# Kernel tuning notes

Measured on AMD Instinct MI355X. Metric: run time of the kernel, lower is better.

Reference implementation:

```python
import jax, jax.numpy as jnp
import numpy as np

CH = 16
R = 9  # reduced_res = ceil(log2(256)+1)


def grid_sample_bilinear(P, gx, gy):
    """torch.F.grid_sample, mode=bilinear, align_corners=True, zeros padding.
    P: (C, H, W); gx indexes width (last axis), gy indexes height. Returns (C, N)."""
    C, H, W = P.shape
    ix = (gx + 1.0) * 0.5 * (W - 1)
    iy = (gy + 1.0) * 0.5 * (H - 1)
    x0 = jnp.floor(ix)
    y0 = jnp.floor(iy)
    wx = ix - x0
    wy = iy - y0
    x0i = jnp.clip(x0.astype(jnp.int32), 0, W - 1)
    x1i = jnp.clip(x0i + 1, 0, W - 1)
    y0i = jnp.clip(y0.astype(jnp.int32), 0, H - 1)
    y1i = jnp.clip(y0i + 1, 0, H - 1)
    v00 = P[:, y0i, x0i]
    v01 = P[:, y0i, x1i]
    v10 = P[:, y1i, x0i]
    v11 = P[:, y1i, x1i]
    return (v00 * (1 - wx) * (1 - wy) + v01 * wx * (1 - wy)
            + v10 * (1 - wx) * wy + v11 * wx * wy)


def plane_feature(P, gx, gy, c_int):
    # sample -> (N, ch, R), then cosine-basis numerical integration over R
    s = grid_sample_bilinear(P, gx, gy)              # (R*ch, N)
    s = s.T.reshape(-1, CH, R)                       # (N, ch, R)
    c = (c_int + 1.0) * 0.5 * (2.0 ** (R - 1) - 1.0)  # (N,)
    freqs = (2.0 ** jnp.arange(R, dtype=jnp.float32)) - 0.5
    basis = jnp.cos(jnp.pi * (c[:, None] + 0.5) * freqs / (2.0 ** R))  # (N, R)
    return 2.0 * jnp.einsum('nr,ncr->nc', basis, s)  # (N, ch)


def setup_inputs() -> dict:
    key = jax.random.key(0)
    k1, k2, k3, k4 = jax.random.split(key, 4)
    coords = jax.random.uniform(k1, (524288, 3), dtype=jnp.float32) * 2.0 - 1.0
    Pu = jax.random.normal(k2, (R * CH, 256, 256), dtype=jnp.float32) * 0.1
    Pv = jax.random.normal(k3, (R * CH, 256, 256), dtype=jnp.float32) * 0.1
    Pw = jax.random.normal(k4, (R * CH, 256, 256), dtype=jnp.float32) * 0.1
    return {"coords": coords, "Pu": Pu, "Pv": Pv, "Pw": Pw}


def reference(coords, Pu, Pv, Pw):
    # Pu sampled with (coord1, coord2), integrated along coord0; etc.
    fu = plane_feature(Pu, coords[:, 1], coords[:, 2], coords[:, 0])
    fv = plane_feature(Pv, coords[:, 0], coords[:, 2], coords[:, 1])
    fw = plane_feature(Pw, coords[:, 0], coords[:, 1], coords[:, 2])
    return fu + fv + fw  # (N, ch)
```

## Files before the change

### kernel.cpp

```cpp
#include <hip/hip_runtime.h>
#include <hip/hip_bf16.h>

#define CHN 16
#define RF 9
#define HWDIM 256
#define POSN (HWDIM * HWDIM)
#define NBINS 32768

__device__ __forceinline__ float bflo(uint32_t v) { return __uint_as_float(v << 16); }
__device__ __forceinline__ float bfhi(uint32_t v) { return __uint_as_float(v & 0xffff0000u); }

__device__ __forceinline__ uint32_t f32_to_bf16(float f) {
    uint32_t u = __float_as_uint(f);
    u += 0x7fffu + ((u >> 16) & 1u);
    return u >> 16;
}

__global__ __launch_bounds__(256) void transpose_pack2(const float* __restrict__ Pu,
                                                       const float* __restrict__ Pv,
                                                       const float* __restrict__ Pw,
                                                       uint4* __restrict__ A,
                                                       uint32_t* __restrict__ B) {
    int tid = blockIdx.x * blockDim.x + threadIdx.x;
    int pos = tid & (POSN - 1);
    int p = tid >> 16;
    const float* P = (p == 0) ? Pu : ((p == 1) ? Pv : Pw);
    uint32_t r8[8];
    uint4* Ap = A + ((size_t)p * POSN + pos) * CHN;
#pragma unroll
    for (int cc = 0; cc < CHN; ++cc) {
        const float* Pc = P + (size_t)(cc * RF) * POSN + pos;
        uint32_t w[4];
#pragma unroll
        for (int j = 0; j < 4; ++j) {
            float v0 = Pc[(size_t)(2 * j) * POSN];
            float v1 = Pc[(size_t)(2 * j + 1) * POSN];
            w[j] = f32_to_bf16(v0) | (f32_to_bf16(v1) << 16);
        }
        Ap[cc] = make_uint4(w[0], w[1], w[2], w[3]);
        uint32_t b8 = f32_to_bf16(Pc[(size_t)8 * POSN]);
        if (cc & 1) r8[cc >> 1] |= (b8 << 16); else r8[cc >> 1] = b8;
    }
    uint32_t* Bp = B + ((size_t)p * POSN + pos) * 8;
#pragma unroll
    for (int j = 0; j < 8; ++j) Bp[j] = r8[j];
}

__device__ __forceinline__ uint32_t part1by2(uint32_t x) {
    x &= 0x3ffu;
    x = (x | (x << 16)) & 0x030000FFu;
    x = (x | (x << 8))  & 0x0300F00Fu;
    x = (x | (x << 4))  & 0x030C30C3u;
    x = (x | (x << 2))  & 0x09249249u;
    return x;
}
__device__ __forceinline__ uint32_t morton_key(float c0, float c1, float c2) {
    int q0 = min(31, max(0, (int)((c0 + 1.f) * 16.f)));
    int q1 = min(31, max(0, (int)((c1 + 1.f) * 16.f)));
    int q2 = min(31, max(0, (int)((c2 + 1.f) * 16.f)));
    return (part1by2((uint32_t)q0) << 2) | (part1by2((uint32_t)q1) << 1) | part1by2((uint32_t)q2);
}

__global__ __launch_bounds__(256) void hist_kernel(const float* __restrict__ coords,
                                                   uint32_t* __restrict__ hist, int N) {
    int n = blockIdx.x * blockDim.x + threadIdx.x;
    if (n >= N) return;
    float c0 = coords[3 * n], c1 = coords[3 * n + 1], c2 = coords[3 * n + 2];
    atomicAdd(&hist[morton_key(c0, c1, c2)], 1u);
}

__global__ __launch_bounds__(1024) void scan_kernel(uint32_t* __restrict__ hist) {
    __shared__ uint32_t part[1024];
    int t = threadIdx.x;
    uint32_t loc[32];
    uint32_t s = 0;
    int base = t * 32;
#pragma unroll
    for (int i = 0; i < 32; ++i) { loc[i] = hist[base + i]; s += loc[i]; }
    part[t] = s;
    __syncthreads();
    for (int off = 1; off < 1024; off <<= 1) {
        uint32_t v = (t >= off) ? part[t - off] : 0u;
        __syncthreads();
        part[t] += v;
        __syncthreads();
    }
    uint32_t run = part[t] - s;
#pragma unroll
    for (int i = 0; i < 32; ++i) { hist[base + i] = run; run += loc[i]; }
}

__global__ __launch_bounds__(256) void scatter_kernel(const float* __restrict__ coords,
                                                      uint32_t* __restrict__ hist,
                                                      float4* __restrict__ sorted, int N) {
    int n = blockIdx.x * blockDim.x + threadIdx.x;
    if (n >= N) return;
    float c0 = coords[3 * n], c1 = coords[3 * n + 1], c2 = coords[3 * n + 2];
    uint32_t key = morton_key(c0, c1, c2);
    uint32_t dst = atomicAdd(&hist[key], 1u);
    sorted[dst] = make_float4(c0, c1, c2, __uint_as_float((uint32_t)n));
}

__global__ __launch_bounds__(256) void triplane_sorted(const float4* __restrict__ sorted,
                                                       const uint4* __restrict__ A,
                                                       const uint32_t* __restrict__ B,
                                                       float* __restrict__ out, int N, int nblk) {
    __shared__ float bas[16][27];
    __shared__ float4 pts[16];
    int blk = blockIdx.x;
    if ((nblk & 7) == 0) {
        int cpx = nblk >> 3;
        blk = (blk & 7) * cpx + (blk >> 3);
    }
    int base = blk * 16;
    int t = threadIdx.x;
    if (t < 16) {
        int i = base + t;
        pts[t] = (i < N) ? sorted[i] : make_float4(0.f, 0.f, 0.f, __uint_as_float(0u));
    }
    __syncthreads();
    if (t < 144) {
        int pt = t / 9, r = t - pt * 9;
        float4 c = pts[pt];
        float k = 3.14159265358979f * ((float)(1 << r) - 0.5f) * (1.f / 512.f);
        bas[pt][0 * 9 + r] = __cosf(((c.x + 1.f) * 127.5f + 0.5f) * k);
        bas[pt][1 * 9 + r] = __cosf(((c.y + 1.f) * 127.5f + 0.5f) * k);
        bas[pt][2 * 9 + r] = __cosf(((c.z + 1.f) * 127.5f + 0.5f) * k);
    }
    __syncthreads();
    int pt = t >> 4, cc = t & 15;
    int gi = base + pt;
    if (gi >= N) return;
    float4 c = pts[pt];
    float acc = 0.f;
#pragma unroll
    for (int p = 0; p < 3; ++p) {
        float gx = (p == 0) ? c.y : c.x;
        float gy = (p == 2) ? c.y : c.z;
        float ix = (gx + 1.f) * 127.5f;
        float iy = (gy + 1.f) * 127.5f;
        float x0f = floorf(ix), y0f = floorf(iy);
        float wx = ix - x0f, wy = iy - y0f;
        int x0 = (int)x0f; x0 = max(0, min(x0, HWDIM - 1));
        int y0 = (int)y0f; y0 = max(0, min(y0, HWDIM - 1));
        int x1 = min(x0 + 1, HWDIM - 1);
        int y1 = min(y0 + 1, HWDIM - 1);
        float b[9];
#pragma unroll
        for (int r = 0; r < 9; ++r) b[r] = bas[pt][p * 9 + r];
        const uint4* Ap = A + (size_t)p * POSN * CHN;
        const uint32_t* Bp = B + (size_t)p * POSN * 8;
        int pos4[4] = { y0 * HWDIM + x0, y0 * HWDIM + x1, y1 * HWDIM + x0, y1 * HWDIM + x1 };
        float w4[4] = { (1.f - wx) * (1.f - wy), wx * (1.f - wy), (1.f - wx) * wy, wx * wy };
        float ps = 0.f;
#pragma unroll
        for (int k = 0; k < 4; ++k) {
            uint4 a = Ap[(size_t)pos4[k] * CHN + cc];
            uint32_t bw = Bp[(size_t)pos4[k] * 8 + (cc >> 1)];
            float s;
            s = b[0] * bflo(a.x);          s = fmaf(b[1], bfhi(a.x), s);
            s = fmaf(b[2], bflo(a.y), s);  s = fmaf(b[3], bfhi(a.y), s);
            s = fmaf(b[4], bflo(a.z), s);  s = fmaf(b[5], bfhi(a.z), s);
            s = fmaf(b[6], bflo(a.w), s);  s = fmaf(b[7], bfhi(a.w), s);
            float v8 = (cc & 1) ? bfhi(bw) : bflo(bw);
            s = fmaf(b[8], v8, s);
            ps = fmaf(w4[k], s, ps);
        }
        acc += ps;
    }
    uint32_t n = __float_as_uint(c.w);
    out[(size_t)n * CHN + cc] = 2.f * acc;
}

__global__ __launch_bounds__(256) void triplane_direct(const float* __restrict__ coords,
                                                       const float* __restrict__ Pu,
                                                       const float* __restrict__ Pv,
                                                       const float* __restrict__ Pw,
                                                       float* __restrict__ out, int N) {
    int tid = blockIdx.x * blockDim.x + threadIdx.x;
    int n = tid >> 4;
    if (n >= N) return;
    int cc = tid & 15;
    float c0 = coords[3 * n + 0];
    float c1 = coords[3 * n + 1];
    float c2 = coords[3 * n + 2];
    float acc = 0.f;
#pragma unroll
    for (int p = 0; p < 3; ++p) {
        const float* P = (p == 0) ? Pu : ((p == 1) ? Pv : Pw);
        float gx = (p == 0) ? c1 : c0;
        float gy = (p == 2) ? c1 : c2;
        float ci = (p == 0) ? c0 : ((p == 1) ? c1 : c2);
        float ix = (gx + 1.f) * 127.5f;
        float iy = (gy + 1.f) * 127.5f;
        float x0f = floorf(ix), y0f = floorf(iy);
        float wx = ix - x0f, wy = iy - y0f;
        int x0 = (int)x0f; x0 = max(0, min(x0, HWDIM - 1));
        int y0 = (int)y0f; y0 = max(0, min(y0, HWDIM - 1));
        int x1 = min(x0 + 1, HWDIM - 1);
        int y1 = min(y0 + 1, HWDIM - 1);
        float cv = (ci + 1.f) * 127.5f + 0.5f;
        float w00 = (1.f - wx) * (1.f - wy), w01 = wx * (1.f - wy);
        float w10 = (1.f - wx) * wy, w11 = wx * wy;
        int p00 = y0 * HWDIM + x0, p01 = y0 * HWDIM + x1;
        int p10 = y1 * HWDIM + x0, p11 = y1 * HWDIM + x1;
#pragma unroll
        for (int r = 0; r < RF; ++r) {
            const float k = 3.14159265358979f * ((float)(1 << r) - 0.5f) / 512.f;
            float b = __cosf(cv * k);
            const float* Pc = P + (size_t)(cc * RF + r) * POSN;
            float v = w00 * Pc[p00] + w01 * Pc[p01] + w10 * Pc[p10] + w11 * Pc[p11];
            acc = fmaf(b, v, acc);
        }
    }
    out[(size_t)n * CHN + cc] = 2.f * acc;
}

extern "C" void kernel_launch(void* const* d_in, const int* in_sizes, int n_in,
                              void* d_out, int out_size, void* d_ws, size_t ws_size,
                              hipStream_t stream) {
    const float* coords = (const float*)d_in[0];
    const float* Pu = (const float*)d_in[1];
    const float* Pv = (const float*)d_in[2];
    const float* Pw = (const float*)d_in[3];
    float* out = (float*)d_out;
    int N = in_sizes[0] / 3;

    size_t offA = 0;
    size_t szA = (size_t)3 * POSN * CHN * sizeof(uint4);
    size_t offB = offA + szA;
    size_t szB = (size_t)3 * POSN * 8 * sizeof(uint32_t);
    size_t offS = offB + szB;
    size_t szS = (size_t)N * sizeof(float4);
    size_t offH = offS + szS;
    size_t szH = (size_t)NBINS * sizeof(uint32_t);
    size_t need = offH + szH;

    if (ws_size >= need) {
        char* ws = (char*)d_ws;
        uint4* A = (uint4*)(ws + offA);
        uint32_t* B = (uint32_t*)(ws + offB);
        float4* sorted = (float4*)(ws + offS);
        uint32_t* hist = (uint32_t*)(ws + offH);

        transpose_pack2<<<(3 * POSN) / 256, 256, 0, stream>>>(Pu, Pv, Pw, A, B);

        hipMemsetAsync(hist, 0, szH, stream);
        hist_kernel<<<(N + 255) / 256, 256, 0, stream>>>(coords, hist, N);
        scan_kernel<<<1, 1024, 0, stream>>>(hist);
        scatter_kernel<<<(N + 255) / 256, 256, 0, stream>>>(coords, hist, sorted, N);

        int nblk = (N + 15) / 16;
        triplane_sorted<<<nblk, 256, 0, stream>>>(sorted, A, B, out, N, nblk);
    } else {
        int threads = N * CHN;
        triplane_direct<<<(threads + 255) / 256, 256, 0, stream>>>(coords, Pu, Pv, Pw, out, N);
    }
}
```

Measured before the change: 193.5 us.

## Pack planes as fp16, use dot2, merge prep kernels, precompute per-point metadata

Changes the packed plane format from bf16 to fp16 so the inner product over the 8 frequency terms can use the packed fp16 dot2 instruction instead of separate unpack and FMA steps. The transpose/pack and histogram kernels are merged into one launch to cut launch overhead and let the two run side by side. Per-point, per-plane bilinear weights, byte offsets and half-precision basis values are computed once into shared memory rather than redundantly by all 16 channel threads. fp16 has a narrower exponent range than bf16, and the basis values are now also rounded to fp16, which slightly changes accuracy.

Measured after the change: 172.0 us. 1.12x faster.

```diff
diff --git a/kernel.cpp b/kernel.cpp
--- a/kernel.cpp
+++ b/kernel.cpp
@@ -7,44 +7,27 @@
 #define POSN (HWDIM * HWDIM)
 #define NBINS 32768
 
-__device__ __forceinline__ float bflo(uint32_t v) { return __uint_as_float(v << 16); }
-__device__ __forceinline__ float bfhi(uint32_t v) { return __uint_as_float(v & 0xffff0000u); }
-
-__device__ __forceinline__ uint32_t f32_to_bf16(float f) {
-    uint32_t u = __float_as_uint(f);
-    u += 0x7fffu + ((u >> 16) & 1u);
-    return u >> 16;
-}
-
-__global__ __launch_bounds__(256) void transpose_pack2(const float* __restrict__ Pu,
-                                                       const float* __restrict__ Pv,
-                                                       const float* __restrict__ Pw,
-                                                       uint4* __restrict__ A,
-                                                       uint32_t* __restrict__ B) {
-    int tid = blockIdx.x * blockDim.x + threadIdx.x;
-    int pos = tid & (POSN - 1);
-    int p = tid >> 16;
-    const float* P = (p == 0) ? Pu : ((p == 1) ? Pv : Pw);
-    uint32_t r8[8];
-    uint4* Ap = A + ((size_t)p * POSN + pos) * CHN;
-#pragma unroll
-    for (int cc = 0; cc < CHN; ++cc) {
-        const float* Pc = P + (size_t)(cc * RF) * POSN + pos;
-        uint32_t w[4];
-#pragma unroll
-        for (int j = 0; j < 4; ++j) {
-            float v0 = Pc[(size_t)(2 * j) * POSN];
-            float v1 = Pc[(size_t)(2 * j + 1) * POSN];
-            w[j] = f32_to_bf16(v0) | (f32_to_bf16(v1) << 16);
-        }
-        Ap[cc] = make_uint4(w[0], w[1], w[2], w[3]);
-        uint32_t b8 = f32_to_bf16(Pc[(size_t)8 * POSN]);
-        if (cc & 1) r8[cc >> 1] |= (b8 << 16); else r8[cc >> 1] = b8;
-    }
-    uint32_t* Bp = B + ((size_t)p * POSN + pos) * 8;
-#pragma unroll
-    for (int j = 0; j < 8; ++j) Bp[j] = r8[j];
-}
+typedef _Float16 half2_t __attribute__((ext_vector_type(2)));
+
+__device__ __forceinline__ half2_t u2h(uint32_t u) {
+    union { uint32_t u; half2_t h; } x; x.u = u; return x.h;
+}
+__device__ __forceinline__ uint32_t f2h(float f) {
+    union { _Float16 h; uint16_t u; } x; x.h = (_Float16)f; return (uint32_t)x.u;
+}
+__device__ __forceinline__ float h2f(uint32_t u) {
+    union { uint16_t u; _Float16 h; } x; x.u = (uint16_t)u; return (float)x.h;
+}
+
+#if __has_builtin(__builtin_amdgcn_fdot2)
+__device__ __forceinline__ float DOT2(half2_t a, half2_t b, float c) {
+    return __builtin_amdgcn_fdot2(a, b, c, false);
+}
+#else
+__device__ __forceinline__ float DOT2(half2_t a, half2_t b, float c) {
+    return fmaf((float)a.x, (float)b.x, fmaf((float)a.y, (float)b.y, c));
+}
+#endif
 
 __device__ __forceinline__ uint32_t part1by2(uint32_t x) {
     x &= 0x3ffu;
@@ -61,12 +44,46 @@
     return (part1by2((uint32_t)q0) << 2) | (part1by2((uint32_t)q1) << 1) | part1by2((uint32_t)q2);
 }
 
-__global__ __launch_bounds__(256) void hist_kernel(const float* __restrict__ coords,
-                                                   uint32_t* __restrict__ hist, int N) {
-    int n = blockIdx.x * blockDim.x + threadIdx.x;
-    if (n >= N) return;
-    float c0 = coords[3 * n], c1 = coords[3 * n + 1], c2 = coords[3 * n + 2];
-    atomicAdd(&hist[morton_key(c0, c1, c2)], 1u);
+__global__ __launch_bounds__(256) void prep_kernel(const float* __restrict__ Pu,
+                                                   const float* __restrict__ Pv,
+                                                   const float* __restrict__ Pw,
+                                                   uint4* __restrict__ A,
+                                                   uint32_t* __restrict__ B,
+                                                   const float* __restrict__ coords,
+                                                   uint32_t* __restrict__ hist,
+                                                   int N, int tblk) {
+    int b = blockIdx.x;
+    if (b < tblk) {
+        int tid = b * 256 + threadIdx.x;
+        int pos = tid & (POSN - 1);
+        int p = tid >> 16;
+        const float* P = (p == 0) ? Pu : ((p == 1) ? Pv : Pw);
+        uint32_t r8pk[8];
+        uint4* Ap = A + ((size_t)p * POSN + pos) * CHN;
+#pragma unroll
+        for (int cc = 0; cc < CHN; ++cc) {
+            const float* Pc = P + (size_t)(cc * RF) * POSN + pos;
+            uint32_t w[4];
+#pragma unroll
+            for (int j = 0; j < 4; ++j) {
+                float v0 = Pc[(size_t)(2 * j) * POSN];
+                float v1 = Pc[(size_t)(2 * j + 1) * POSN];
+                w[j] = f2h(v0) | (f2h(v1) << 16);
+            }
+            Ap[cc] = make_uint4(w[0], w[1], w[2], w[3]);
+            uint32_t h8 = f2h(Pc[(size_t)8 * POSN]);
+            if (cc & 1) r8pk[cc >> 1] |= (h8 << 16); else r8pk[cc >> 1] = h8;
+        }
+        uint32_t* Bp = B + ((size_t)p * POSN + pos) * 8;
+#pragma unroll
+        for (int j = 0; j < 8; ++j) Bp[j] = r8pk[j];
+    } else {
+        int n = (b - tblk) * 256 + threadIdx.x;
+        if (n < N) {
+            float c0 = coords[3 * n], c1 = coords[3 * n + 1], c2 = coords[3 * n + 2];
+            atomicAdd(&hist[morton_key(c0, c1, c2)], 1u);
+        }
+    }
 }
 
 __global__ __launch_bounds__(1024) void scan_kernel(uint32_t* __restrict__ hist) {
@@ -101,12 +118,12 @@
     sorted[dst] = make_float4(c0, c1, c2, __uint_as_float((uint32_t)n));
 }
 
-__global__ __launch_bounds__(256) void triplane_sorted(const float4* __restrict__ sorted,
-                                                       const uint4* __restrict__ A,
-                                                       const uint32_t* __restrict__ B,
-                                                       float* __restrict__ out, int N, int nblk) {
-    __shared__ float bas[16][27];
+__global__ __launch_bounds__(256) void triplane_f16(const float4* __restrict__ sorted,
+                                                    const uint4* __restrict__ A,
+                                                    const uint32_t* __restrict__ B,
+                                                    float* __restrict__ out, int N, int nblk) {
     __shared__ float4 pts[16];
+    __shared__ uint32_t meta[16][3][16];
     int blk = blockIdx.x;
     if ((nblk & 7) == 0) {
         int cpx = nblk >> 3;
@@ -119,56 +136,71 @@
         pts[t] = (i < N) ? sorted[i] : make_float4(0.f, 0.f, 0.f, __uint_as_float(0u));
     }
     __syncthreads();
-    if (t < 144) {
-        int pt = t / 9, r = t - pt * 9;
+    if (t < 64 && (t & 3) < 3) {
+        int pt = t >> 2, p = t & 3;
         float4 c = pts[pt];
-        float k = 3.14159265358979f * ((float)(1 << r) - 0.5f) * (1.f / 512.f);
-        bas[pt][0 * 9 + r] = __cosf(((c.x + 1.f) * 127.5f + 0.5f) * k);
-        bas[pt][1 * 9 + r] = __cosf(((c.y + 1.f) * 127.5f + 0.5f) * k);
-        bas[pt][2 * 9 + r] = __cosf(((c.z + 1.f) * 127.5f + 0.5f) * k);
+        float gx = (p == 0) ? c.y : c.x;
+        float gy = (p == 2) ? c.y : c.z;
+        float ci = (p == 0) ? c.x : ((p == 1) ? c.y : c.z);
+        float ix = (gx + 1.f) * 127.5f;
+        float iy = (gy + 1.f) * 127.5f;
+        float x0f = floorf(ix), y0f = floorf(iy);
+        float wx = ix - x0f, wy = iy - y0f;
+        int x0 = min(max((int)x0f, 0), HWDIM - 1);
+        int y0 = min(max((int)y0f, 0), HWDIM - 1);
+        int x1 = min(x0 + 1, HWDIM - 1);
+        int y1 = min(y0 + 1, HWDIM - 1);
+        uint32_t* m = meta[pt][p];
+        float cv = (ci + 1.f) * 127.5f + 0.5f;
+        float bb[9];
+#pragma unroll
+        for (int r = 0; r < 9; ++r) {
+            const float k = 3.14159265358979f * ((float)(1 << r) - 0.5f) * (1.f / 512.f);
+            bb[r] = __cosf(cv * k);
+        }
+#pragma unroll
+        for (int j = 0; j < 4; ++j) m[j] = f2h(bb[2 * j]) | (f2h(bb[2 * j + 1]) << 16);
+        m[4] = __float_as_uint(bb[8]);
+        m[5] = __float_as_uint((1.f - wx) * (1.f - wy));
+        m[6] = __float_as_uint(wx * (1.f - wy));
+        m[7] = __float_as_uint((1.f - wx) * wy);
+        m[8] = __float_as_uint(wx * wy);
+        m[9]  = (uint32_t)(y0 * HWDIM + x0) * 256u;
+        m[10] = (uint32_t)(y0 * HWDIM + x1) * 256u;
+        m[11] = (uint32_t)(y1 * HWDIM + x0) * 256u;
+        m[12] = (uint32_t)(y1 * HWDIM + x1) * 256u;
     }
     __syncthreads();
     int pt = t >> 4, cc = t & 15;
     int gi = base + pt;
     if (gi >= N) return;
-    float4 c = pts[pt];
     float acc = 0.f;
+    const char* Ab = (const char*)A;
+    const char* Bb = (const char*)B;
 #pragma unroll
     for (int p = 0; p < 3; ++p) {
-        float gx = (p == 0) ? c.y : c.x;
-        float gy = (p == 2) ? c.y : c.z;
-        float ix = (gx + 1.f) * 127.5f;
-        float iy = (gy + 1.f) * 127.5f;
-        float x0f = floorf(ix), y0f = floorf(iy);
-        float wx = ix - x0f, wy = iy - y0f;
-        int x0 = (int)x0f; x0 = max(0, min(x0, HWDIM - 1));
-        int y0 = (int)y0f; y0 = max(0, min(y0, HWDIM - 1));
-        int x1 = min(x0 + 1, HWDIM - 1);
-        int y1 = min(y0 + 1, HWDIM - 1);
-        float b[9];
-#pragma unroll
-        for (int r = 0; r < 9; ++r) b[r] = bas[pt][p * 9 + r];
-        const uint4* Ap = A + (size_t)p * POSN * CHN;
-        const uint32_t* Bp = B + (size_t)p * POSN * 8;
-        int pos4[4] = { y0 * HWDIM + x0, y0 * HWDIM + x1, y1 * HWDIM + x0, y1 * HWDIM + x1 };
-        float w4[4] = { (1.f - wx) * (1.f - wy), wx * (1.f - wy), (1.f - wx) * wy, wx * wy };
+        const uint32_t* m = meta[pt][p];
+        half2_t b01 = u2h(m[0]), b23 = u2h(m[1]), b45 = u2h(m[2]), b67 = u2h(m[3]);
+        float b8 = __uint_as_float(m[4]);
+        const char* Apl = Ab + (size_t)p * ((size_t)POSN * 256);
+        const char* Bpl = Bb + (size_t)p * ((size_t)POSN * 32);
         float ps = 0.f;
 #pragma unroll
         for (int k = 0; k < 4; ++k) {
-            uint4 a = Ap[(size_t)pos4[k] * CHN + cc];
-            uint32_t bw = Bp[(size_t)pos4[k] * 8 + (cc >> 1)];
-            float s;
-            s = b[0] * bflo(a.x);          s = fmaf(b[1], bfhi(a.x), s);
-            s = fmaf(b[2], bflo(a.y), s);  s = fmaf(b[3], bfhi(a.y), s);
-            s = fmaf(b[4], bflo(a.z), s);  s = fmaf(b[5], bfhi(a.z), s);
-            s = fmaf(b[6], bflo(a.w), s);  s = fmaf(b[7], bfhi(a.w), s);
-            float v8 = (cc & 1) ? bfhi(bw) : bflo(bw);
-            s = fmaf(b[8], v8, s);
-            ps = fmaf(w4[k], s, ps);
+            uint32_t ob = m[9 + k];
+            uint4 a = *(const uint4*)(Apl + ob + cc * 16);
+            uint32_t bw = *(const uint32_t*)(Bpl + (ob >> 3) + ((cc >> 1) << 2));
+            float v8 = h2f((cc & 1) ? (bw >> 16) : (bw & 0xffffu));
+            float s = b8 * v8;
+            s = DOT2(u2h(a.x), b01, s);
+            s = DOT2(u2h(a.y), b23, s);
+            s = DOT2(u2h(a.z), b45, s);
+            s = DOT2(u2h(a.w), b67, s);
+            ps = fmaf(__uint_as_float(m[5 + k]), s, ps);
         }
         acc += ps;
     }
-    uint32_t n = __float_as_uint(c.w);
+    uint32_t n = __float_as_uint(pts[pt].w);
     out[(size_t)n * CHN + cc] = 2.f * acc;
 }
 
@@ -195,8 +227,8 @@
         float iy = (gy + 1.f) * 127.5f;
         float x0f = floorf(ix), y0f = floorf(iy);
         float wx = ix - x0f, wy = iy - y0f;
-        int x0 = (int)x0f; x0 = max(0, min(x0, HWDIM - 1));
-        int y0 = (int)y0f; y0 = max(0, min(y0, HWDIM - 1));
+        int x0 = min(max((int)x0f, 0), HWDIM - 1);
+        int y0 = min(max((int)y0f, 0), HWDIM - 1);
         int x1 = min(x0 + 1, HWDIM - 1);
         int y1 = min(y0 + 1, HWDIM - 1);
         float cv = (ci + 1.f) * 127.5f + 0.5f;
@@ -243,15 +275,15 @@
         float4* sorted = (float4*)(ws + offS);
         uint32_t* hist = (uint32_t*)(ws + offH);
 
-        transpose_pack2<<<(3 * POSN) / 256, 256, 0, stream>>>(Pu, Pv, Pw, A, B);
-
         hipMemsetAsync(hist, 0, szH, stream);
-        hist_kernel<<<(N + 255) / 256, 256, 0, stream>>>(coords, hist, N);
+        int tblk = (3 * POSN) / 256;
+        int hblk = (N + 255) / 256;
+        prep_kernel<<<tblk + hblk, 256, 0, stream>>>(Pu, Pv, Pw, A, B, coords, hist, N, tblk);
         scan_kernel<<<1, 1024, 0, stream>>>(hist);
         scatter_kernel<<<(N + 255) / 256, 256, 0, stream>>>(coords, hist, sorted, N);
 
         int nblk = (N + 15) / 16;
-        triplane_sorted<<<nblk, 256, 0, stream>>>(sorted, A, B, out, N, nblk);
+        triplane_f16<<<nblk, 256, 0, stream>>>(sorted, A, B, out, N, nblk);
     } else {
         int threads = N * CHN;
         triplane_direct<<<(threads + 255) / 256, 256, 0, stream>>>(coords, Pu, Pv, Pw, out, N);
```
